# Optimization experiments

Hardware: AMD Instinct MI355X
Metric: run time of the kernel (lower is better)

## Reference

```python
import jax, jax.numpy as jnp
import numpy as np

EMBED_DIM = 512
NUM_TYPES = 26
PER_TYPE = 128
NUM_CODES = NUM_TYPES * PER_TYPE
COMMIT = 0.25
TEMP = 0.07
N_TOKENS = 32768
SAMPLED_PER_TYPE = int(0.1 * PER_TYPE)  # 12


def _normalize(v, axis=-1):
    # matches F.normalize(p=2) with eps clamp
    return v / jnp.clip(jnp.linalg.norm(v, axis=axis, keepdims=True), 1e-12)


def setup_inputs() -> dict:
    key = jax.random.key(0)
    k1, k2, k3, k4 = jax.random.split(key, 4)
    x = jax.random.normal(k1, (N_TOKENS, EMBED_DIM), jnp.float32)
    Q = jax.random.randint(k2, (N_TOKENS,), 0, NUM_TYPES)
    initrange = 1.0 / EMBED_DIM
    emb = jax.random.uniform(k3, (NUM_CODES, EMBED_DIM), jnp.float32, -initrange, initrange)
    emb = _normalize(emb)  # mirrors _initialize_embeddings
    # deterministic stand-in for torch.randperm(num_per_type)[:sampled_num]
    perm = jax.random.permutation(k4, PER_TYPE)[:SAMPLED_PER_TYPE]
    sampled_indices = (jnp.arange(NUM_TYPES)[:, None] * PER_TYPE + perm[None, :]).reshape(-1)
    return {"x": x, "embeddings": emb, "Q": Q, "sampled_indices": sampled_indices}


def _code_indices(xn, embeddings, Q):
    # full [N, num_codes] squared distances, then select the 128-code slab of
    # each token's PTM type and argmin within it (equivalent to the per-type loop)
    d = ((xn ** 2).sum(-1, keepdims=True)
         + (embeddings ** 2).sum(-1)[None, :]
         - 2.0 * (xn @ embeddings.T))                      # [N, NUM_CODES]
    d = d.reshape(xn.shape[0], NUM_TYPES, PER_TYPE)
    d_sel = jnp.take_along_axis(d, Q[:, None, None], axis=1)[:, 0, :]  # [N, PER_TYPE]
    return jnp.argmin(d_sel, axis=1) + Q * PER_TYPE


def _uniform_loss(embeddings, sampled_indices):
    ne = _normalize(embeddings)
    se = ne[sampled_indices]                               # [S, D]
    sim = se @ se.T                                        # [S, S]
    labels = sampled_indices // PER_TYPE
    pos = (labels[None, :] == labels[:, None]).astype(jnp.float32)
    S = sampled_indices.shape[0]
    eye = jnp.eye(S, dtype=bool)
    sim = jnp.where(eye, -jnp.inf, sim)
    sim_exp = jnp.exp(sim / TEMP)                          # exp(-inf) = 0 kills diagonal
    sum_exp = sim_exp.sum(axis=1)
    pos_sum = (sim_exp * pos).sum(axis=1)
    return -jnp.log(pos_sum / sum_exp).mean()


def reference(x, embeddings, Q, sampled_indices):
    xn = _normalize(x)
    idx = _code_indices(xn, embeddings, Q)
    quantized = _normalize(embeddings[idx])
    q_latent = jnp.mean((quantized - jax.lax.stop_gradient(xn)) ** 2)
    e_latent = jnp.mean((xn - jax.lax.stop_gradient(quantized)) ** 2)
    loss = q_latent + COMMIT * e_latent
    uloss = _uniform_loss(embeddings, sampled_indices)
    out = xn + jax.lax.stop_gradient(quantized - xn)       # straight-through
    return out, loss, uloss, idx
```

## Files before the change

### kernel.cpp

```cpp
#include <hip/hip_runtime.h>
#include <math.h>

#define NTOK   32768
#define DIM    512
#define NTYPES 26
#define PT     128
#define NCODES 3328
#define NSAMP  312
#define INV_TEMP (1.0f / 0.07f)
#define MAXTILES 24

typedef __attribute__((ext_vector_type(8))) short short8;
typedef __attribute__((ext_vector_type(4))) float floatx4;

__device__ __forceinline__ void f2bf2(float f, unsigned short& h, unsigned short& l) {
    unsigned u = __float_as_uint(f);
    unsigned hb = (u + 0x7fffu + ((u >> 16) & 1u)) >> 16;
    h = (unsigned short)hb;
    float hf = __uint_as_float(hb << 16);
    float r = f - hf;
    unsigned u2 = __float_as_uint(r);
    l = (unsigned short)((u2 + 0x7fffu + ((u2 >> 16) & 1u)) >> 16);
}

__global__ __launch_bounds__(256) void k_emb(const float* __restrict__ emb,
                                             unsigned short* __restrict__ Bhg,
                                             unsigned short* __restrict__ Blg,
                                             float* __restrict__ sume,
                                             float* __restrict__ rinv,
                                             int* __restrict__ counts,
                                             float* __restrict__ accg) {
    int tid = threadIdx.x;
    if (blockIdx.x == 0) {
        if (tid < NTYPES) counts[tid] = 0;
        if (tid == 32) accg[0] = 0.0f;
        if (tid == 33) accg[1] = 0.0f;
    }
    int wv = tid >> 6, lane = tid & 63;
    int c = blockIdx.x * 4 + wv;
    const float4* row = (const float4*)(emb + (size_t)c * DIM);
    float4 v0 = row[lane * 2], v1 = row[lane * 2 + 1];
    float s = v0.x*v0.x + v0.y*v0.y + v0.z*v0.z + v0.w*v0.w
            + v1.x*v1.x + v1.y*v1.y + v1.z*v1.z + v1.w*v1.w;
    for (int m = 32; m; m >>= 1) s += __shfl_xor(s, m);
    if (lane == 0) {
        sume[c] = s;
        rinv[c] = 1.0f / fmaxf(sqrtf(s), 1e-12f);
    }
    union { short8 v; unsigned short u[8]; } hh, ll;
    f2bf2(v0.x, hh.u[0], ll.u[0]); f2bf2(v0.y, hh.u[1], ll.u[1]);
    f2bf2(v0.z, hh.u[2], ll.u[2]); f2bf2(v0.w, hh.u[3], ll.u[3]);
    f2bf2(v1.x, hh.u[4], ll.u[4]); f2bf2(v1.y, hh.u[5], ll.u[5]);
    f2bf2(v1.z, hh.u[6], ll.u[6]); f2bf2(v1.w, hh.u[7], ll.u[7]);
    int qq  = c >> 7;
    int n   = c & 127;
    int ni  = n >> 4, lcc = n & 15;
    int ks2 = lane >> 2, q4d = lane & 3;
    size_t dst = (size_t)qq * (PT * DIM)
               + (size_t)(((ks2 * 8 + ni) * 64 + q4d * 16 + lcc) * 8);
    *(short8*)(Bhg + dst) = hh.v;
    *(short8*)(Blg + dst) = ll.v;
}

__global__ __launch_bounds__(256) void k_hist(const int* __restrict__ Q,
                                              int* __restrict__ counts,
                                              int* __restrict__ rank) {
    __shared__ int lbin[NTYPES];
    __shared__ int lbase[NTYPES];
    int tid = threadIdx.x;
    if (tid < NTYPES) lbin[tid] = 0;
    __syncthreads();
    int t = blockIdx.x * 256 + tid;
    int qt = Q[t];
    int lr = atomicAdd(&lbin[qt], 1);
    __syncthreads();
    if (tid < NTYPES) lbase[tid] = atomicAdd(&counts[tid], lbin[tid]);
    __syncthreads();
    rank[t] = lbase[qt] + lr;
}

__global__ __launch_bounds__(256) void k_scatter(const int* __restrict__ Q,
                                                 const int* __restrict__ counts,
                                                 const int* __restrict__ rank,
                                                 int* __restrict__ order,
                                                 int* __restrict__ offsg) {
    __shared__ int offs[NTYPES];
    int tid = threadIdx.x;
    if (tid == 0) {
        int a = 0;
        for (int i = 0; i < NTYPES; i++) {
            offs[i] = a;
            if (blockIdx.x == 0) offsg[i] = a;
            a += counts[i];
        }
        if (blockIdx.x == 0) offsg[NTYPES] = a;
    }
    __syncthreads();
    int t = blockIdx.x * 256 + tid;
    order[offs[Q[t]] + rank[t]] = t;
}

__global__ __launch_bounds__(256, 4) void k_main(const float* __restrict__ x,
                                                 const float* __restrict__ emb,
                                                 const unsigned short* __restrict__ Bhg,
                                                 const unsigned short* __restrict__ Blg,
                                                 const int* __restrict__ order,
                                                 const int* __restrict__ offsg,
                                                 const float* __restrict__ sume,
                                                 const float* __restrict__ rinv,
                                                 float* __restrict__ outbuf,
                                                 float* __restrict__ idxout,
                                                 float* __restrict__ accg) {
    int q = blockIdx.x;
    int base = offsg[q];
    int cnt = offsg[q + 1] - base;
    int wv = threadIdx.x >> 6;
    int tstart = blockIdx.y * 64 + wv * 16;
    if (tstart >= cnt) return;
    int ntw = min(16, cnt - tstart);

    int lane = threadIdx.x & 63;
    int lc = lane & 15, q4 = lane >> 4;

    int tok = order[base + tstart + min(lc, ntw - 1)];
    const float* ap = x + (size_t)tok * DIM + q4 * 8;

    const unsigned short* bh = Bhg + (size_t)q * (PT * DIM) + lane * 8;
    const unsigned short* bl = Blg + (size_t)q * (PT * DIM) + lane * 8;

    float sv[8];
#pragma unroll
    for (int ni = 0; ni < 8; ni++) sv[ni] = sume[q * PT + ni * 16 + lc];

    floatx4 acc[8];
#pragma unroll
    for (int i = 0; i < 8; i++) acc[i] = (floatx4){0.f, 0.f, 0.f, 0.f};
    float ps = 0.0f;

    for (int ks2 = 0; ks2 < 16; ks2++) {
        float4 a0 = *(const float4*)(ap);
        float4 a1 = *(const float4*)(ap + 4);
        ap += 32;
        ps = fmaf(a0.x, a0.x, fmaf(a0.y, a0.y, fmaf(a0.z, a0.z, fmaf(a0.w, a0.w, ps))));
        ps = fmaf(a1.x, a1.x, fmaf(a1.y, a1.y, fmaf(a1.z, a1.z, fmaf(a1.w, a1.w, ps))));
        union { short8 v; unsigned short u[8]; } ah, al;
        f2bf2(a0.x, ah.u[0], al.u[0]); f2bf2(a0.y, ah.u[1], al.u[1]);
        f2bf2(a0.z, ah.u[2], al.u[2]); f2bf2(a0.w, ah.u[3], al.u[3]);
        f2bf2(a1.x, ah.u[4], al.u[4]); f2bf2(a1.y, ah.u[5], al.u[5]);
        f2bf2(a1.z, ah.u[6], al.u[6]); f2bf2(a1.w, ah.u[7], al.u[7]);

        const unsigned short* bkh = bh + ks2 * 4096;
        const unsigned short* bkl = bl + ks2 * 4096;
#pragma unroll
        for (int h = 0; h < 2; h++) {
            short8 bhf[4], blf[4];
#pragma unroll
            for (int j = 0; j < 4; j++) {
                bhf[j] = *(const short8*)(bkh + (h * 4 + j) * 512);
                blf[j] = *(const short8*)(bkl + (h * 4 + j) * 512);
            }
#pragma unroll
            for (int j = 0; j < 4; j++) {
                acc[h * 4 + j] = __builtin_amdgcn_mfma_f32_16x16x32_bf16(ah.v, bhf[j], acc[h * 4 + j], 0, 0, 0);
                acc[h * 4 + j] = __builtin_amdgcn_mfma_f32_16x16x32_bf16(ah.v, blf[j], acc[h * 4 + j], 0, 0, 0);
                acc[h * 4 + j] = __builtin_amdgcn_mfma_f32_16x16x32_bf16(al.v, bhf[j], acc[h * 4 + j], 0, 0, 0);
            }
        }
    }

    ps += __shfl_xor(ps, 16);
    ps += __shfl_xor(ps, 32);
    float rnv = 1.0f / fmaxf(sqrtf(ps), 1e-12f);

    float termsum = 0.0f;
    int bca[4];
#pragma unroll
    for (int r = 0; r < 4; r++) {
        int row = q4 * 4 + r;
        float rn2 = -2.0f * __shfl(rnv, row);
        float bv = 1e30f; int bc = 0;
#pragma unroll
        for (int ni = 0; ni < 8; ni++) {
            float d = fmaf(rn2, acc[ni][r], sv[ni]);
            int n = ni * 16 + lc;
            if (d < bv) { bv = d; bc = n; }
        }
#pragma unroll
        for (int mk = 1; mk <= 8; mk <<= 1) {
            float ov = __shfl_xor(bv, mk);
            int oc = __shfl_xor(bc, mk);
            if (ov < bv || (ov == bv && oc < bc)) { bv = ov; bc = oc; }
        }
        bca[r] = bc;
        int gt = __shfl(tok, row);
        if (lc == 0 && row < ntw) {
            idxout[gt] = (float)(q * PT + bc);
            float se = sume[q * PT + bc];
            float rc = rinv[q * PT + bc];
            termsum += 2.0f - (se - bv) * rc;
        }
    }
    termsum += __shfl_xor(termsum, 16);
    termsum += __shfl_xor(termsum, 32);
    if (lane == 0) atomicAdd(&accg[0], termsum);

#pragma unroll
    for (int g = 0; g < 4; g++) {
#pragma unroll
        for (int r = 0; r < 4; r++) {
            int row = g * 4 + r;
            if (row >= ntw) continue;
            int c = __shfl(bca[r], g * 16);
            int gt = __shfl(tok, row);
            float rv = rinv[q * PT + c];
            const float4* er = (const float4*)(emb + (size_t)(q * PT + c) * DIM);
            float4* orow = (float4*)(outbuf + (size_t)gt * DIM);
            float4 e0 = er[lane * 2], e1 = er[lane * 2 + 1];
            orow[lane * 2]     = make_float4(e0.x * rv, e0.y * rv, e0.z * rv, e0.w * rv);
            orow[lane * 2 + 1] = make_float4(e1.x * rv, e1.y * rv, e1.z * rv, e1.w * rv);
        }
    }
}

__global__ __launch_bounds__(256) void k_uloss(const float* __restrict__ emb,
                                               const int* __restrict__ samp,
                                               const float* __restrict__ rinv,
                                               float* __restrict__ accg) {
    __shared__ float rs[4], rp[4];
    int i = blockIdx.x;
    int tid = threadIdx.x;
    int lane = tid & 63, wv = tid >> 6;
    int ci = samp[i];
    float rvi = rinv[ci];
    int labi = ci >> 7;
    const float4* ri = (const float4*)(emb + (size_t)ci * DIM);
    float4 e0 = ri[lane * 2], e1 = ri[lane * 2 + 1];
    float sE = 0.0f, pE = 0.0f;
    for (int j0 = wv; j0 < NSAMP; j0 += 16) {
        float d[4]; int cj[4]; bool val[4];
#pragma unroll
        for (int u = 0; u < 4; u++) {
            int j = j0 + u * 4;
            val[u] = (j < NSAMP) && (j != i);
            int js = val[u] ? j : 0;
            cj[u] = samp[js];
            const float4* rj = (const float4*)(emb + (size_t)cj[u] * DIM);
            float4 f0 = rj[lane * 2], f1 = rj[lane * 2 + 1];
            d[u] = e0.x*f0.x + e0.y*f0.y + e0.z*f0.z + e0.w*f0.w
                 + e1.x*f1.x + e1.y*f1.y + e1.z*f1.z + e1.w*f1.w;
        }
#pragma unroll
        for (int mk = 32; mk; mk >>= 1)
#pragma unroll
            for (int u = 0; u < 4; u++) d[u] += __shfl_xor(d[u], mk);
#pragma unroll
        for (int u = 0; u < 4; u++) {
            float ex = val[u] ? expf(d[u] * rvi * rinv[cj[u]] * INV_TEMP) : 0.0f;
            sE += ex;
            if (val[u] && (cj[u] >> 7) == labi) pE += ex;
        }
    }
    if (lane == 0) { rs[wv] = sE; rp[wv] = pE; }
    __syncthreads();
    if (tid == 0) {
        float S = rs[0] + rs[1] + rs[2] + rs[3];
        float P = rp[0] + rp[1] + rp[2] + rp[3];
        atomicAdd(&accg[1], logf(S) - logf(P));
    }
}

__global__ void k_final(const float* __restrict__ accg, float* __restrict__ lossp) {
    lossp[0] = (1.25f / ((float)NTOK * (float)DIM)) * accg[0];
    lossp[1] = accg[1] / (float)NSAMP;
}

extern "C" void kernel_launch(void* const* d_in, const int* in_sizes, int n_in,
                              void* d_out, int out_size, void* d_ws, size_t ws_size,
                              hipStream_t stream) {
    const float* x   = (const float*)d_in[0];
    const float* emb = (const float*)d_in[1];
    const int* Q     = (const int*)d_in[2];
    const int* samp  = (const int*)d_in[3];

    float* out    = (float*)d_out;
    float* lossp  = out + (size_t)NTOK * DIM;
    float* idxout = out + (size_t)NTOK * DIM + 2;

    unsigned short* Bhg = (unsigned short*)d_ws;
    unsigned short* Blg = Bhg + (size_t)NCODES * DIM;
    float* sume  = (float*)(Blg + (size_t)NCODES * DIM);
    float* rinv  = sume + NCODES;
    int* counts  = (int*)(rinv + NCODES);
    int* offsg   = counts + NTYPES;
    int* rank    = offsg + NTYPES + 1;
    int* order   = rank + NTOK;
    float* accg  = (float*)(order + NTOK);

    k_emb<<<NCODES / 4, 256, 0, stream>>>(emb, Bhg, Blg, sume, rinv, counts, accg);
    k_hist<<<NTOK / 256, 256, 0, stream>>>(Q, counts, rank);
    k_scatter<<<NTOK / 256, 256, 0, stream>>>(Q, counts, rank, order, offsg);
    dim3 gmain(NTYPES, MAXTILES);
    k_main<<<gmain, 256, 0, stream>>>(x, emb, Bhg, Blg, order, offsg, sume, rinv, out, idxout, accg);
    k_uloss<<<NSAMP, 256, 0, stream>>>(emb, samp, rinv, accg);
    k_final<<<1, 1, 0, stream>>>(accg, lossp);
}
```

Baseline: 233.6 us.

## Remap main kernel blocks to XCDs per type and prefetch activations

Changes k_main to a 1D grid in which each block ID is decoded so that all tiles of a given code type land on the same XCD (bid & 7). The intent is that a type's bf16 codebook slab stays resident in that XCD's L2. It also software-prefetches the token activations two k-steps ahead, issues all eight B fragment loads per k-step at once, and fully unrolls the k loop. Launch bounds drop to 3 waves per SIMD, allowing more registers for the deeper prefetch. The risks are lower occupancy and load imbalance across XCDs, since 26 types do not split evenly over 8.

```diff
diff --git a/kernel.cpp b/kernel.cpp
--- a/kernel.cpp
+++ b/kernel.cpp
@@ -100,7 +100,7 @@
     order[offs[Q[t]] + rank[t]] = t;
 }
 
-__global__ __launch_bounds__(256, 4) void k_main(const float* __restrict__ x,
+__global__ __launch_bounds__(256, 3) void k_main(const float* __restrict__ x,
                                                  const float* __restrict__ emb,
                                                  const unsigned short* __restrict__ Bhg,
                                                  const unsigned short* __restrict__ Blg,
@@ -111,11 +111,18 @@
                                                  float* __restrict__ outbuf,
                                                  float* __restrict__ idxout,
                                                  float* __restrict__ accg) {
-    int q = blockIdx.x;
+    int bid = blockIdx.x;
+    int xcd = bid & 7;
+    int slot = bid >> 3;
+    int jt = slot / MAXTILES;
+    int tile = slot - jt * MAXTILES;
+    int q = xcd + 8 * jt;
+    if (q >= NTYPES) return;
+
     int base = offsg[q];
     int cnt = offsg[q + 1] - base;
     int wv = threadIdx.x >> 6;
-    int tstart = blockIdx.y * 64 + wv * 16;
+    int tstart = tile * 64 + wv * 16;
     if (tstart >= cnt) return;
     int ntw = min(16, cnt - tstart);
 
@@ -123,7 +130,7 @@
     int lc = lane & 15, q4 = lane >> 4;
 
     int tok = order[base + tstart + min(lc, ntw - 1)];
-    const float* ap = x + (size_t)tok * DIM + q4 * 8;
+    const float4* fa = (const float4*)(x + (size_t)tok * DIM) + q4 * 2;
 
     const unsigned short* bh = Bhg + (size_t)q * (PT * DIM) + lane * 8;
     const unsigned short* bl = Blg + (size_t)q * (PT * DIM) + lane * 8;
@@ -137,10 +144,26 @@
     for (int i = 0; i < 8; i++) acc[i] = (floatx4){0.f, 0.f, 0.f, 0.f};
     float ps = 0.0f;
 
+    float4 pa0[2], pa1[2];
+    pa0[0] = fa[0];  pa1[0] = fa[1];
+    pa0[1] = fa[8];  pa1[1] = fa[9];
+
+#pragma unroll
     for (int ks2 = 0; ks2 < 16; ks2++) {
-        float4 a0 = *(const float4*)(ap);
-        float4 a1 = *(const float4*)(ap + 4);
-        ap += 32;
+        int cur = ks2 & 1;
+        const unsigned short* bkh = bh + ks2 * 4096;
+        const unsigned short* bkl = bl + ks2 * 4096;
+        short8 bhf[8], blf[8];
+#pragma unroll
+        for (int j2 = 0; j2 < 8; j2++) {
+            bhf[j2] = *(const short8*)(bkh + j2 * 512);
+            blf[j2] = *(const short8*)(bkl + j2 * 512);
+        }
+        float4 a0 = pa0[cur], a1 = pa1[cur];
+        if (ks2 < 14) {
+            pa0[cur] = fa[(ks2 + 2) * 8];
+            pa1[cur] = fa[(ks2 + 2) * 8 + 1];
+        }
         ps = fmaf(a0.x, a0.x, fmaf(a0.y, a0.y, fmaf(a0.z, a0.z, fmaf(a0.w, a0.w, ps))));
         ps = fmaf(a1.x, a1.x, fmaf(a1.y, a1.y, fmaf(a1.z, a1.z, fmaf(a1.w, a1.w, ps))));
         union { short8 v; unsigned short u[8]; } ah, al;
@@ -148,23 +171,11 @@
         f2bf2(a0.z, ah.u[2], al.u[2]); f2bf2(a0.w, ah.u[3], al.u[3]);
         f2bf2(a1.x, ah.u[4], al.u[4]); f2bf2(a1.y, ah.u[5], al.u[5]);
         f2bf2(a1.z, ah.u[6], al.u[6]); f2bf2(a1.w, ah.u[7], al.u[7]);
-
-        const unsigned short* bkh = bh + ks2 * 4096;
-        const unsigned short* bkl = bl + ks2 * 4096;
-#pragma unroll
-        for (int h = 0; h < 2; h++) {
-            short8 bhf[4], blf[4];
-#pragma unroll
-            for (int j = 0; j < 4; j++) {
-                bhf[j] = *(const short8*)(bkh + (h * 4 + j) * 512);
-                blf[j] = *(const short8*)(bkl + (h * 4 + j) * 512);
-            }
-#pragma unroll
-            for (int j = 0; j < 4; j++) {
-                acc[h * 4 + j] = __builtin_amdgcn_mfma_f32_16x16x32_bf16(ah.v, bhf[j], acc[h * 4 + j], 0, 0, 0);
-                acc[h * 4 + j] = __builtin_amdgcn_mfma_f32_16x16x32_bf16(ah.v, blf[j], acc[h * 4 + j], 0, 0, 0);
-                acc[h * 4 + j] = __builtin_amdgcn_mfma_f32_16x16x32_bf16(al.v, bhf[j], acc[h * 4 + j], 0, 0, 0);
-            }
+#pragma unroll
+        for (int j2 = 0; j2 < 8; j2++) {
+            acc[j2] = __builtin_amdgcn_mfma_f32_16x16x32_bf16(ah.v, bhf[j2], acc[j2], 0, 0, 0);
+            acc[j2] = __builtin_amdgcn_mfma_f32_16x16x32_bf16(ah.v, blf[j2], acc[j2], 0, 0, 0);
+            acc[j2] = __builtin_amdgcn_mfma_f32_16x16x32_bf16(al.v, bhf[j2], acc[j2], 0, 0, 0);
         }
     }
 
@@ -299,8 +310,7 @@
     k_emb<<<NCODES / 4, 256, 0, stream>>>(emb, Bhg, Blg, sume, rinv, counts, accg);
     k_hist<<<NTOK / 256, 256, 0, stream>>>(Q, counts, rank);
     k_scatter<<<NTOK / 256, 256, 0, stream>>>(Q, counts, rank, order, offsg);
-    dim3 gmain(NTYPES, MAXTILES);
-    k_main<<<gmain, 256, 0, stream>>>(x, emb, Bhg, Blg, order, offsg, sume, rinv, out, idxout, accg);
+    k_main<<<8 * 96, 256, 0, stream>>>(x, emb, Bhg, Blg, order, offsg, sume, rinv, out, idxout, accg);
     k_uloss<<<NSAMP, 256, 0, stream>>>(emb, samp, rinv, accg);
     k_final<<<1, 1, 0, stream>>>(accg, lossp);
 }
```

New measurement: 239.7 us. +2.6%, slower.

## Share codebook tiles via LDS double-buffering across a 2x2 wave grid in k_main

Applied to the files above, without the earlier changes.

The main distance kernel is restructured so the four waves of a block form a 2x2 grid over 64 tokens and 128 codes. Before, each wave handled 16 tokens against all 128 codes and loaded the bf16 hi/lo codebook straight from global memory. Now the codebook slices are staged into double-buffered LDS with global_load_lds, and x loads are software-pipelined one K-step ahead under explicit waitcnt and barriers. The per-wave argmin halves are combined through shared memory, and the occupancy hint drops from 4 to 3 blocks to make room for the extra LDS and registers. The aim is to cut redundant global and L2 traffic for the codebook, at the cost of block-level barriers every K-step.

```diff
diff --git a/kernel.cpp b/kernel.cpp
--- a/kernel.cpp
+++ b/kernel.cpp
@@ -21,6 +21,22 @@
     float r = f - hf;
     unsigned u2 = __float_as_uint(r);
     l = (unsigned short)((u2 + 0x7fffu + ((u2 >> 16) & 1u)) >> 16);
+}
+
+__device__ __forceinline__ void cvt8(float4 a, float4 b, short8& h, short8& l) {
+    union { short8 v; unsigned short u[8]; } H, L;
+    f2bf2(a.x, H.u[0], L.u[0]); f2bf2(a.y, H.u[1], L.u[1]);
+    f2bf2(a.z, H.u[2], L.u[2]); f2bf2(a.w, H.u[3], L.u[3]);
+    f2bf2(b.x, H.u[4], L.u[4]); f2bf2(b.y, H.u[5], L.u[5]);
+    f2bf2(b.z, H.u[6], L.u[6]); f2bf2(b.w, H.u[7], L.u[7]);
+    h = H.v; l = L.v;
+}
+
+__device__ __forceinline__ void stage2(const unsigned short* g, unsigned short* l) {
+    __builtin_amdgcn_global_load_lds((const __attribute__((address_space(1))) void*)g,
+                                     (__attribute__((address_space(3))) void*)l, 16, 0, 0);
+    __builtin_amdgcn_global_load_lds((const __attribute__((address_space(1))) void*)(g + 512),
+                                     (__attribute__((address_space(3))) void*)(l + 512), 16, 0, 0);
 }
 
 __global__ __launch_bounds__(256) void k_emb(const float* __restrict__ emb,
@@ -100,7 +116,51 @@
     order[offs[Q[t]] + rank[t]] = t;
 }
 
-__global__ __launch_bounds__(256, 4) void k_main(const float* __restrict__ x,
+#define KSTEP(S, NSTR, AC, AN, RESTAGE, LOADA)                                   \
+  {                                                                              \
+    __builtin_amdgcn_sched_barrier(0);                                           \
+    asm volatile("s_waitcnt vmcnt(" NSTR ")" ::: "memory");                      \
+    __builtin_amdgcn_s_barrier();                                                \
+    __builtin_amdgcn_sched_barrier(0);                                           \
+    if (RESTAGE) {                                                               \
+      stage2(bhg + ((S) + 1) * 4096 + stoff, &Bls[((S) + 1) & 1][0][ldoff]);     \
+      stage2(blg + ((S) + 1) * 4096 + stoff, &Bls[((S) + 1) & 1][1][ldoff]);     \
+    }                                                                            \
+    __builtin_amdgcn_sched_barrier(0);                                           \
+    if (LOADA) {                                                                 \
+      AN[0] = *(const float4*)(ap0 + ((S) + 1) * 32);                            \
+      AN[1] = *(const float4*)(ap0 + ((S) + 1) * 32 + 4);                        \
+      AN[2] = *(const float4*)(ap1 + ((S) + 1) * 32);                            \
+      AN[3] = *(const float4*)(ap1 + ((S) + 1) * 32 + 4);                        \
+    }                                                                            \
+    {                                                                            \
+      float4 r0a = AC[0], r0b = AC[1], r1a = AC[2], r1b = AC[3];                 \
+      ps0 = fmaf(r0a.x, r0a.x, fmaf(r0a.y, r0a.y, fmaf(r0a.z, r0a.z, fmaf(r0a.w, r0a.w, ps0)))); \
+      ps0 = fmaf(r0b.x, r0b.x, fmaf(r0b.y, r0b.y, fmaf(r0b.z, r0b.z, fmaf(r0b.w, r0b.w, ps0)))); \
+      ps1 = fmaf(r1a.x, r1a.x, fmaf(r1a.y, r1a.y, fmaf(r1a.z, r1a.z, fmaf(r1a.w, r1a.w, ps1)))); \
+      ps1 = fmaf(r1b.x, r1b.x, fmaf(r1b.y, r1b.y, fmaf(r1b.z, r1b.z, fmaf(r1b.w, r1b.w, ps1)))); \
+      short8 ah0, al0, ah1, al1;                                                 \
+      cvt8(r0a, r0b, ah0, al0);                                                  \
+      cvt8(r1a, r1b, ah1, al1);                                                  \
+      short8 bhf[4], blf[4];                                                     \
+      _Pragma("unroll")                                                          \
+      for (int ni = 0; ni < 4; ni++) {                                           \
+        bhf[ni] = *(const short8*)&Bls[(S) & 1][0][(wn4 + ni) * 512 + lane8];    \
+        blf[ni] = *(const short8*)&Bls[(S) & 1][1][(wn4 + ni) * 512 + lane8];    \
+      }                                                                          \
+      _Pragma("unroll")                                                          \
+      for (int ni = 0; ni < 4; ni++) {                                           \
+        acc[0][ni] = __builtin_amdgcn_mfma_f32_16x16x32_bf16(ah0, bhf[ni], acc[0][ni], 0, 0, 0); \
+        acc[0][ni] = __builtin_amdgcn_mfma_f32_16x16x32_bf16(ah0, blf[ni], acc[0][ni], 0, 0, 0); \
+        acc[0][ni] = __builtin_amdgcn_mfma_f32_16x16x32_bf16(al0, bhf[ni], acc[0][ni], 0, 0, 0); \
+        acc[1][ni] = __builtin_amdgcn_mfma_f32_16x16x32_bf16(ah1, bhf[ni], acc[1][ni], 0, 0, 0); \
+        acc[1][ni] = __builtin_amdgcn_mfma_f32_16x16x32_bf16(ah1, blf[ni], acc[1][ni], 0, 0, 0); \
+        acc[1][ni] = __builtin_amdgcn_mfma_f32_16x16x32_bf16(al1, bhf[ni], acc[1][ni], 0, 0, 0); \
+      }                                                                          \
+    }                                                                            \
+  }
+
+__global__ __launch_bounds__(256, 3) void k_main(const float* __restrict__ x,
                                                  const float* __restrict__ emb,
                                                  const unsigned short* __restrict__ Bhg,
                                                  const unsigned short* __restrict__ Blg,
@@ -112,112 +172,137 @@
                                                  float* __restrict__ idxout,
                                                  float* __restrict__ accg) {
     int q = blockIdx.x;
+    int tile = blockIdx.y;
     int base = offsg[q];
     int cnt = offsg[q + 1] - base;
-    int wv = threadIdx.x >> 6;
-    int tstart = blockIdx.y * 64 + wv * 16;
+    int tstart = tile * 64;
     if (tstart >= cnt) return;
-    int ntw = min(16, cnt - tstart);
-
-    int lane = threadIdx.x & 63;
+    int nt = min(64, cnt - tstart);
+
+    __shared__ unsigned short Bls[2][2][4096];
+    __shared__ int   toks_s[64];
+    __shared__ float sume_s[128];
+    __shared__ float rinv_s[128];
+    __shared__ float redv[64][2];
+    __shared__ int   redi[64][2];
+    __shared__ int   bestc[64];
+
+    int tid = threadIdx.x;
+    int lane = tid & 63;
+    int wv = tid >> 6;
+    int wm = wv & 1, wn = wv >> 1;
     int lc = lane & 15, q4 = lane >> 4;
-
-    int tok = order[base + tstart + min(lc, ntw - 1)];
-    const float* ap = x + (size_t)tok * DIM + q4 * 8;
-
-    const unsigned short* bh = Bhg + (size_t)q * (PT * DIM) + lane * 8;
-    const unsigned short* bl = Blg + (size_t)q * (PT * DIM) + lane * 8;
-
-    float sv[8];
-#pragma unroll
-    for (int ni = 0; ni < 8; ni++) sv[ni] = sume[q * PT + ni * 16 + lc];
-
-    floatx4 acc[8];
-#pragma unroll
-    for (int i = 0; i < 8; i++) acc[i] = (floatx4){0.f, 0.f, 0.f, 0.f};
-    float ps = 0.0f;
-
-    for (int ks2 = 0; ks2 < 16; ks2++) {
-        float4 a0 = *(const float4*)(ap);
-        float4 a1 = *(const float4*)(ap + 4);
-        ap += 32;
-        ps = fmaf(a0.x, a0.x, fmaf(a0.y, a0.y, fmaf(a0.z, a0.z, fmaf(a0.w, a0.w, ps))));
-        ps = fmaf(a1.x, a1.x, fmaf(a1.y, a1.y, fmaf(a1.z, a1.z, fmaf(a1.w, a1.w, ps))));
-        union { short8 v; unsigned short u[8]; } ah, al;
-        f2bf2(a0.x, ah.u[0], al.u[0]); f2bf2(a0.y, ah.u[1], al.u[1]);
-        f2bf2(a0.z, ah.u[2], al.u[2]); f2bf2(a0.w, ah.u[3], al.u[3]);
-        f2bf2(a1.x, ah.u[4], al.u[4]); f2bf2(a1.y, ah.u[5], al.u[5]);
-        f2bf2(a1.z, ah.u[6], al.u[6]); f2bf2(a1.w, ah.u[7], al.u[7]);
-
-        const unsigned short* bkh = bh + ks2 * 4096;
-        const unsigned short* bkl = bl + ks2 * 4096;
-#pragma unroll
-        for (int h = 0; h < 2; h++) {
-            short8 bhf[4], blf[4];
-#pragma unroll
-            for (int j = 0; j < 4; j++) {
-                bhf[j] = *(const short8*)(bkh + (h * 4 + j) * 512);
-                blf[j] = *(const short8*)(bkl + (h * 4 + j) * 512);
+    int wn4 = wn * 4, lane8 = lane * 8;
+    int stoff = wv * 1024 + lane8;
+    int ldoff = wv * 1024;
+
+    if (tid < 64) toks_s[tid] = order[base + tstart + min(tid, nt - 1)];
+    if (tid < 128) {
+        sume_s[tid] = sume[q * PT + tid];
+        rinv_s[tid] = rinv[q * PT + tid];
+    }
+
+    int row0 = wm * 32 + lc;
+    int tok0 = order[base + tstart + min(row0, nt - 1)];
+    int tok1 = order[base + tstart + min(row0 + 16, nt - 1)];
+    const float* ap0 = x + (size_t)tok0 * DIM + q4 * 8;
+    const float* ap1 = x + (size_t)tok1 * DIM + q4 * 8;
+
+    const unsigned short* bhg = Bhg + (size_t)q * (PT * DIM);
+    const unsigned short* blg = Blg + (size_t)q * (PT * DIM);
+
+    floatx4 acc[2][4];
+#pragma unroll
+    for (int mi = 0; mi < 2; mi++)
+#pragma unroll
+        for (int ni = 0; ni < 4; ni++)
+            acc[mi][ni] = (floatx4){0.f, 0.f, 0.f, 0.f};
+    float ps0 = 0.f, ps1 = 0.f;
+    float4 Aa[4], Ab[4];
+
+    stage2(bhg + stoff, &Bls[0][0][ldoff]);
+    stage2(blg + stoff, &Bls[0][1][ldoff]);
+    __builtin_amdgcn_sched_barrier(0);
+    Aa[0] = *(const float4*)(ap0);     Aa[1] = *(const float4*)(ap0 + 4);
+    Aa[2] = *(const float4*)(ap1);     Aa[3] = *(const float4*)(ap1 + 4);
+    __builtin_amdgcn_sched_barrier(0);
+    stage2(bhg + 4096 + stoff, &Bls[1][0][ldoff]);
+    stage2(blg + 4096 + stoff, &Bls[1][1][ldoff]);
+    asm volatile("s_waitcnt lgkmcnt(0)" ::: "memory");
+
+    KSTEP(0,  "8", Aa, Ab, 0, 1)
+    KSTEP(1,  "4", Ab, Aa, 1, 1)
+    KSTEP(2,  "4", Aa, Ab, 1, 1)
+    KSTEP(3,  "4", Ab, Aa, 1, 1)
+    KSTEP(4,  "4", Aa, Ab, 1, 1)
+    KSTEP(5,  "4", Ab, Aa, 1, 1)
+    KSTEP(6,  "4", Aa, Ab, 1, 1)
+    KSTEP(7,  "4", Ab, Aa, 1, 1)
+    KSTEP(8,  "4", Aa, Ab, 1, 1)
+    KSTEP(9,  "4", Ab, Aa, 1, 1)
+    KSTEP(10, "4", Aa, Ab, 1, 1)
+    KSTEP(11, "4", Ab, Aa, 1, 1)
+    KSTEP(12, "4", Aa, Ab, 1, 1)
+    KSTEP(13, "4", Ab, Aa, 1, 1)
+    KSTEP(14, "4", Aa, Ab, 1, 1)
+    KSTEP(15, "4", Ab, Aa, 0, 0)
+
+    ps0 += __shfl_xor(ps0, 16); ps0 += __shfl_xor(ps0, 32);
+    ps1 += __shfl_xor(ps1, 16); ps1 += __shfl_xor(ps1, 32);
+    float rn0 = 1.0f / fmaxf(sqrtf(ps0), 1e-12f);
+    float rn1 = 1.0f / fmaxf(sqrtf(ps1), 1e-12f);
+
+#pragma unroll
+    for (int mi = 0; mi < 2; mi++) {
+#pragma unroll
+        for (int r = 0; r < 4; r++) {
+            int rowrel = q4 * 4 + r;
+            float rn = __shfl(mi == 0 ? rn0 : rn1, rowrel);
+            float rn2v = -2.0f * rn;
+            float bv = 1e30f; int bc = 0;
+#pragma unroll
+            for (int ni = 0; ni < 4; ni++) {
+                int n = wn * 64 + ni * 16 + lc;
+                float d = fmaf(rn2v, acc[mi][ni][r], sume_s[n]);
+                if (d < bv) { bv = d; bc = n; }
             }
 #pragma unroll
-            for (int j = 0; j < 4; j++) {
-                acc[h * 4 + j] = __builtin_amdgcn_mfma_f32_16x16x32_bf16(ah.v, bhf[j], acc[h * 4 + j], 0, 0, 0);
-                acc[h * 4 + j] = __builtin_amdgcn_mfma_f32_16x16x32_bf16(ah.v, blf[j], acc[h * 4 + j], 0, 0, 0);
-                acc[h * 4 + j] = __builtin_amdgcn_mfma_f32_16x16x32_bf16(al.v, bhf[j], acc[h * 4 + j], 0, 0, 0);
+            for (int mk = 1; mk <= 8; mk <<= 1) {
+                float ov = __shfl_xor(bv, mk);
+                int oc = __shfl_xor(bc, mk);
+                if (ov < bv || (ov == bv && oc < bc)) { bv = ov; bc = oc; }
             }
-        }
-    }
-
-    ps += __shfl_xor(ps, 16);
-    ps += __shfl_xor(ps, 32);
-    float rnv = 1.0f / fmaxf(sqrtf(ps), 1e-12f);
-
-    float termsum = 0.0f;
-    int bca[4];
-#pragma unroll
-    for (int r = 0; r < 4; r++) {
-        int row = q4 * 4 + r;
-        float rn2 = -2.0f * __shfl(rnv, row);
-        float bv = 1e30f; int bc = 0;
-#pragma unroll
-        for (int ni = 0; ni < 8; ni++) {
-            float d = fmaf(rn2, acc[ni][r], sv[ni]);
-            int n = ni * 16 + lc;
-            if (d < bv) { bv = d; bc = n; }
-        }
-#pragma unroll
-        for (int mk = 1; mk <= 8; mk <<= 1) {
-            float ov = __shfl_xor(bv, mk);
-            int oc = __shfl_xor(bc, mk);
-            if (ov < bv || (ov == bv && oc < bc)) { bv = ov; bc = oc; }
-        }
-        bca[r] = bc;
-        int gt = __shfl(tok, row);
-        if (lc == 0 && row < ntw) {
-            idxout[gt] = (float)(q * PT + bc);
-            float se = sume[q * PT + bc];
-            float rc = rinv[q * PT + bc];
-            termsum += 2.0f - (se - bv) * rc;
-        }
-    }
-    termsum += __shfl_xor(termsum, 16);
-    termsum += __shfl_xor(termsum, 32);
-    if (lane == 0) atomicAdd(&accg[0], termsum);
-
-#pragma unroll
-    for (int g = 0; g < 4; g++) {
-#pragma unroll
-        for (int r = 0; r < 4; r++) {
-            int row = g * 4 + r;
-            if (row >= ntw) continue;
-            int c = __shfl(bca[r], g * 16);
-            int gt = __shfl(tok, row);
-            float rv = rinv[q * PT + c];
-            const float4* er = (const float4*)(emb + (size_t)(q * PT + c) * DIM);
-            float4* orow = (float4*)(outbuf + (size_t)gt * DIM);
-            float4 e0 = er[lane * 2], e1 = er[lane * 2 + 1];
-            orow[lane * 2]     = make_float4(e0.x * rv, e0.y * rv, e0.z * rv, e0.w * rv);
-            orow[lane * 2 + 1] = make_float4(e1.x * rv, e1.y * rv, e1.z * rv, e1.w * rv);
+            int m = wm * 32 + mi * 16 + rowrel;
+            if (lc == 0) { redv[m][wn] = bv; redi[m][wn] = bc; }
+        }
+    }
+    __syncthreads();
+
+    if (tid < 64) {
+        float v0 = redv[tid][0], v1 = redv[tid][1];
+        int c = (v1 < v0) ? redi[tid][1] : redi[tid][0];
+        float bvv = fminf(v0, v1);
+        bestc[tid] = c;
+        float term = 0.0f;
+        if (tid < nt) {
+            idxout[toks_s[tid]] = (float)(q * PT + c);
+            term = 2.0f - (sume_s[c] - bvv) * rinv_s[c];
+        }
+        for (int mk = 32; mk; mk >>= 1) term += __shfl_xor(term, mk);
+        if (tid == 0) atomicAdd(&accg[0], term);
+    }
+    __syncthreads();
+
+    for (int t = wv; t < nt; t += 4) {
+        int c = bestc[t];
+        int gt = toks_s[t];
+        float rv = rinv_s[c];
+        const float4* er = (const float4*)(emb + (size_t)(q * PT + c) * DIM);
+        float4* orow = (float4*)(outbuf + (size_t)gt * DIM);
+#pragma unroll
+        for (int s2 = 0; s2 < 2; s2++) {
+            float4 ev = er[lane * 2 + s2];
+            orow[lane * 2 + s2] = make_float4(ev.x * rv, ev.y * rv, ev.z * rv, ev.w * rv);
         }
     }
 }
```

New measurement: 209.1 us. -10.5%, faster.
